# Performance work log

Hardware: AMD Instinct MI355X
Metric: run time of the kernel (lower is better)

The kernel has to match this reference:

```python
import jax, jax.numpy as jnp
import numpy as np

HIDDEN = 2048
NUM_HEADS = 16
NUM_KV_HEADS = 8
HEAD_DIM = 128
Q_SIZE = NUM_HEADS * HEAD_DIM          # 2048
KV_SIZE = NUM_KV_HEADS * HEAD_DIM      # 1024
ROPE_THETA = 1000000.0
RMS_EPS = 1e-6
SCALE = HEAD_DIM ** -0.5


def setup_inputs() -> dict:
    key = jax.random.key(0)
    k1, k2, k3 = jax.random.split(key, 3)
    T = 4096
    positions = jnp.arange(T, dtype=jnp.int64) if jax.config.jax_enable_x64 else jnp.arange(T, dtype=jnp.int32)
    hidden_states = jax.random.normal(k1, (T, HIDDEN), dtype=jnp.float32)
    qkv_w = jax.random.normal(k2, (Q_SIZE + 2 * KV_SIZE, HIDDEN), dtype=jnp.float32) * 0.02
    o_w = jax.random.normal(k3, (HIDDEN, Q_SIZE), dtype=jnp.float32) * 0.02
    q_norm_w = jnp.ones((HEAD_DIM,), dtype=jnp.float32)
    k_norm_w = jnp.ones((HEAD_DIM,), dtype=jnp.float32)
    return {
        "hidden_states": hidden_states,
        "qkv_w": qkv_w,
        "q_norm_w": q_norm_w,
        "k_norm_w": k_norm_w,
        "o_w": o_w,
        "positions": positions,
    }


def _rms_norm(x, w, eps=RMS_EPS):
    # per-head RMSNorm over last dim (head_dim)
    var = jnp.mean(jnp.square(x), axis=-1, keepdims=True)
    return x * jax.lax.rsqrt(var + eps) * w


def _rope(x, positions):
    # neox-style (rotate-half) RoPE. x: [T, H, D], positions: [T]
    D = x.shape[-1]
    inv_freq = 1.0 / (ROPE_THETA ** (jnp.arange(0, D, 2, dtype=jnp.float32) / D))  # [D/2]
    freqs = positions.astype(jnp.float32)[:, None] * inv_freq                      # [T, D/2]
    cos = jnp.cos(freqs)[:, None, :]  # [T, 1, D/2]
    sin = jnp.sin(freqs)[:, None, :]
    x1, x2 = x[..., : D // 2], x[..., D // 2 :]
    return jnp.concatenate([x1 * cos - x2 * sin, x2 * cos + x1 * sin], axis=-1)


def reference(hidden_states, qkv_w, q_norm_w, k_norm_w, o_w, positions):
    T = hidden_states.shape[0]
    qkv = hidden_states @ qkv_w.T                                   # [T, Q+2KV]
    q = qkv[:, :Q_SIZE].reshape(T, NUM_HEADS, HEAD_DIM)
    k = qkv[:, Q_SIZE : Q_SIZE + KV_SIZE].reshape(T, NUM_KV_HEADS, HEAD_DIM)
    v = qkv[:, Q_SIZE + KV_SIZE :].reshape(T, NUM_KV_HEADS, HEAD_DIM)

    # attention_bias=False path: per-head QK RMSNorm
    q = _rms_norm(q, q_norm_w)
    k = _rms_norm(k, k_norm_w)

    q = _rope(q, positions)
    k = _rope(k, positions)

    # GQA: expand KV heads to query heads
    rep = NUM_HEADS // NUM_KV_HEADS
    k = jnp.repeat(k, rep, axis=1)   # [T, H, D]
    v = jnp.repeat(v, rep, axis=1)

    scores = jnp.einsum("qhd,khd->hqk", q, k) * SCALE               # [H, T, T]
    causal = positions[:, None] >= positions[None, :]               # [T, T]
    scores = jnp.where(causal[None], scores, jnp.finfo(scores.dtype).min)
    probs = jax.nn.softmax(scores, axis=-1)
    attn = jnp.einsum("hqk,khd->qhd", probs, v)                     # [T, H, D]
    return attn.reshape(T, Q_SIZE) @ o_w.T                          # [T, HIDDEN]
```

## Files before the change

kernel.cpp:

```cpp
#include <hip/hip_runtime.h>
#include <hip/hip_bf16.h>
#include <math.h>


typedef __bf16 bf16;
typedef __bf16 bf16x4 __attribute__((ext_vector_type(4)));
typedef __bf16 bf16x8 __attribute__((ext_vector_type(8)));
typedef float  f32x4  __attribute__((ext_vector_type(4)));

__device__ __forceinline__ f32x4 mfma16(bf16x8 a, bf16x8 b, f32x4 c) {
  return __builtin_amdgcn_mfma_f32_16x16x32_bf16(a, b, c, 0, 0, 0);
}

__device__ __forceinline__ void mfma16x16_chain4(const bf16x4& a0, const bf16x4& a1,
                                                 const bf16x4& a2, const bf16x4& a3,
                                                 const bf16x4& b0, const bf16x4& b1,
                                                 const bf16x4& b2, const bf16x4& b3,
                                                 f32x4& c) {
  asm volatile(
      "s_nop 2\n\t"
      "v_mfma_f32_16x16x16_bf16 %0, %1, %5, %0\n\t"
      "v_mfma_f32_16x16x16_bf16 %0, %2, %6, %0\n\t"
      "v_mfma_f32_16x16x16_bf16 %0, %3, %7, %0\n\t"
      "v_mfma_f32_16x16x16_bf16 %0, %4, %8, %0"
      : "+v"(c)
      : "v"(a0), "v"(a1), "v"(a2), "v"(a3),
        "v"(b0), "v"(b1), "v"(b2), "v"(b3));
}

__device__ __forceinline__ void gload_lds16(const bf16* g, bf16* l) {
  __builtin_amdgcn_global_load_lds(
      (const __attribute__((address_space(1))) unsigned int*)g,
      (__attribute__((address_space(3))) unsigned int*)l, 16, 0, 0);
}

__device__ __forceinline__ void store_c(float* p, float v) { *p = v; }
__device__ __forceinline__ void store_c(bf16* p, float v) { *p = (bf16)v; }

__global__ __launch_bounds__(256) void cast_bf16(const float* __restrict__ s,
                                                 bf16* __restrict__ d) {
  int i = blockIdx.x * 256 + threadIdx.x;
  float4 a = reinterpret_cast<const float4*>(s)[i * 2];
  float4 b = reinterpret_cast<const float4*>(s)[i * 2 + 1];
  bf16x8 v = {(bf16)a.x, (bf16)a.y, (bf16)a.z, (bf16)a.w,
              (bf16)b.x, (bf16)b.y, (bf16)b.z, (bf16)b.w};
  reinterpret_cast<bf16x8*>(d)[i] = v;
}

__global__ __launch_bounds__(512, 2) void gemm8ph(const bf16* __restrict__ A,
                                                  const bf16* __restrict__ B,
                                                  bf16* __restrict__ C,
                                                  int M, int N, int K) {
  __shared__ __align__(16) bf16 As[2][256 * 64];
  __shared__ __align__(16) bf16 Bs[2][256 * 64];

  const int tid  = threadIdx.x;
  const int lane = tid & 63, wid = tid >> 6;
  const int quad = lane >> 4, l16 = lane & 15;
  const int wr = wid >> 2, wc = wid & 3;

  const int nbx = N >> 8;
  const int nwg = (M >> 8) * nbx;
  const int cpx = nwg >> 3;
  const int swz = ((int)blockIdx.x & 7) * cpx + ((int)blockIdx.x >> 3);
  const int m0 = (swz / nbx) << 8;
  const int n0 = (swz % nbx) << 8;

  const int srow = tid >> 3;
  const int scol = (((tid & 7) ^ (srow & 7)) << 3);
  const bf16* aS = &A[(size_t)(m0 + srow) * K + scol];
  const bf16* bS = &B[(size_t)(n0 + srow) * K + scol];
  const size_t rk64 = (size_t)64 * K;

  const int koff0 = ((quad)     ^ (l16 & 7)) << 3;
  const int koff1 = ((4 + quad) ^ (l16 & 7)) << 3;

  const f32x4 zero = {0.f, 0.f, 0.f, 0.f};
  f32x4 acc[8][4];
#pragma unroll
  for (int i = 0; i < 8; ++i)
#pragma unroll
    for (int j = 0; j < 4; ++j) acc[i][j] = zero;

  const int NT = K >> 6;

  {
    gload_lds16(aS,            &As[0][tid * 8]);
    gload_lds16(aS + rk64,     &As[0][4096 + tid * 8]);
    gload_lds16(aS + 2 * rk64, &As[0][8192 + tid * 8]);
    gload_lds16(aS + 3 * rk64, &As[0][12288 + tid * 8]);
    gload_lds16(bS,            &Bs[0][tid * 8]);
    gload_lds16(bS + rk64,     &Bs[0][4096 + tid * 8]);
    gload_lds16(bS + 2 * rk64, &Bs[0][8192 + tid * 8]);
    gload_lds16(bS + 3 * rk64, &Bs[0][12288 + tid * 8]);
  }
  asm volatile("s_waitcnt vmcnt(0)" ::: "memory");
  __builtin_amdgcn_s_barrier();

  for (int t = 0; t < NT; ++t) {
    const int c = t & 1;
    const bf16* AsL = As[c];
    const bf16* BsL = Bs[c];
    const bool pre = (t + 1 < NT);
    const size_t nk = (size_t)(t + 1) * 64;
    bf16* An = As[c ^ 1];
    bf16* Bn = Bs[c ^ 1];

    bf16x8 bfv[4][2];

#pragma unroll
    for (int p = 0; p < 4; ++p) {
      if (p == 0) {
#pragma unroll
        for (int fn = 0; fn < 4; ++fn) {
          const bf16* bp = &BsL[(wc * 64 + fn * 16 + l16) * 64];
          bfv[fn][0] = *reinterpret_cast<const bf16x8*>(&bp[koff0]);
          bfv[fn][1] = *reinterpret_cast<const bf16x8*>(&bp[koff1]);
        }
      }
      const bf16* ap0 = &AsL[(wr * 128 + (2 * p) * 16 + l16) * 64];
      const bf16* ap1 = ap0 + 16 * 64;
      bf16x8 a0k0 = *reinterpret_cast<const bf16x8*>(&ap0[koff0]);
      bf16x8 a0k1 = *reinterpret_cast<const bf16x8*>(&ap0[koff1]);
      bf16x8 a1k0 = *reinterpret_cast<const bf16x8*>(&ap1[koff0]);
      bf16x8 a1k1 = *reinterpret_cast<const bf16x8*>(&ap1[koff1]);

      if (p == 0 && pre) {
        gload_lds16(aS + nk,            &An[tid * 8]);
        gload_lds16(aS + rk64 + nk,     &An[4096 + tid * 8]);
        gload_lds16(aS + 2 * rk64 + nk, &An[8192 + tid * 8]);
        gload_lds16(aS + 3 * rk64 + nk, &An[12288 + tid * 8]);
      }
      if (p == 1 && pre) {
        gload_lds16(bS + nk,            &Bn[tid * 8]);
        gload_lds16(bS + rk64 + nk,     &Bn[4096 + tid * 8]);
        gload_lds16(bS + 2 * rk64 + nk, &Bn[8192 + tid * 8]);
        gload_lds16(bS + 3 * rk64 + nk, &Bn[12288 + tid * 8]);
      }

      __builtin_amdgcn_s_barrier();
      __builtin_amdgcn_sched_barrier(0);

      __builtin_amdgcn_s_setprio(1);
#pragma unroll
      for (int fn = 0; fn < 4; ++fn) {
        acc[2 * p][fn]     = mfma16(a0k1, bfv[fn][1],
                                    mfma16(a0k0, bfv[fn][0], acc[2 * p][fn]));
        acc[2 * p + 1][fn] = mfma16(a1k1, bfv[fn][1],
                                    mfma16(a1k0, bfv[fn][0], acc[2 * p + 1][fn]));
      }
      __builtin_amdgcn_s_setprio(0);

      if (p == 3 && pre) {
        asm volatile("s_waitcnt vmcnt(0)" ::: "memory");
      }
      __builtin_amdgcn_s_barrier();
    }
  }

#pragma unroll
  for (int fm = 0; fm < 8; ++fm)
#pragma unroll
    for (int fn = 0; fn < 4; ++fn)
#pragma unroll
      for (int r = 0; r < 4; ++r) {
        int row = m0 + wr * 128 + fm * 16 + quad * 4 + r;
        int col = n0 + wc * 64 + fn * 16 + l16;
        C[(size_t)row * N + col] = (bf16)acc[fm][fn][r];
      }
}

__device__ __forceinline__ void gemm_step(const bf16* AsL, const bf16* BsL,
                                          int wm, int wn, int l16, int quad,
                                          f32x4 (&acc)[4][4]) {
  bf16x8 af[4], bfr[4];
#pragma unroll
  for (int i = 0; i < 4; ++i)
    af[i] = *reinterpret_cast<const bf16x8*>(&AsL[(wm + i * 16 + l16) * 32 + quad * 8]);
#pragma unroll
  for (int j = 0; j < 4; ++j)
    bfr[j] = *reinterpret_cast<const bf16x8*>(&BsL[(wn + j * 16 + l16) * 32 + quad * 8]);
#pragma unroll
  for (int i = 0; i < 4; ++i)
#pragma unroll
    for (int j = 0; j < 4; ++j)
      acc[i][j] = mfma16(af[i], bfr[j], acc[i][j]);
}

template <typename TC>
__global__ __launch_bounds__(256, 4) void gemm_bt(const bf16* __restrict__ A,
                                                  const bf16* __restrict__ B,
                                                  TC* __restrict__ C,
                                                  int M, int N, int K) {
  __shared__ __align__(16) bf16 As[2][128 * 32];
  __shared__ __align__(16) bf16 Bs[2][128 * 32];

  const int tid  = threadIdx.x;
  const int wave = tid >> 6, lane = tid & 63;
  const int quad = lane >> 4, l16 = lane & 15;
  const int wm = (wave >> 1) * 64, wn = (wave & 1) * 64;
  const int n0 = blockIdx.x * 128, m0 = blockIdx.y * 128;

  const int r0 = tid >> 2;
  const int c0 = (tid & 3) * 8;
  const size_t aBase = (size_t)(m0 + r0) * K + c0;
  const size_t bBase = (size_t)(n0 + r0) * K + c0;
  const size_t rowK64 = (size_t)64 * K;

  const f32x4 zero = {0.f, 0.f, 0.f, 0.f};
  f32x4 acc[4][4];
#pragma unroll
  for (int i = 0; i < 4; ++i)
#pragma unroll
    for (int j = 0; j < 4; ++j) acc[i][j] = zero;

  gload_lds16(&A[aBase],          &As[0][tid * 8]);
  gload_lds16(&A[aBase + rowK64], &As[0][2048 + tid * 8]);
  gload_lds16(&B[bBase],          &Bs[0][tid * 8]);
  gload_lds16(&B[bBase + rowK64], &Bs[0][2048 + tid * 8]);
  __syncthreads();

  int cur = 0;
  for (int k0 = 32; k0 < K; k0 += 32) {
    const int nb = cur ^ 1;
    gload_lds16(&A[aBase + k0],          &As[nb][tid * 8]);
    gload_lds16(&A[aBase + rowK64 + k0], &As[nb][2048 + tid * 8]);
    gload_lds16(&B[bBase + k0],          &Bs[nb][tid * 8]);
    gload_lds16(&B[bBase + rowK64 + k0], &Bs[nb][2048 + tid * 8]);

    gemm_step(As[cur], Bs[cur], wm, wn, l16, quad, acc);

    __syncthreads();
    cur = nb;
  }
  gemm_step(As[cur], Bs[cur], wm, wn, l16, quad, acc);

#pragma unroll
  for (int i = 0; i < 4; ++i)
#pragma unroll
    for (int j = 0; j < 4; ++j)
#pragma unroll
      for (int r = 0; r < 4; ++r) {
        int row = m0 + wm + i * 16 + quad * 4 + r;
        int col = n0 + wn + j * 16 + l16;
        store_c(&C[(size_t)row * N + col], acc[i][j][r]);
      }
}

__global__ __launch_bounds__(256) void norm_rope(const bf16* __restrict__ qkv,
                                                 const float* __restrict__ qw,
                                                 const float* __restrict__ kw,
                                                 const int* __restrict__ pos,
                                                 bf16* __restrict__ qn,
                                                 bf16* __restrict__ kn) {
  const int t = blockIdx.x;
  const int wv = threadIdx.x >> 6, l = threadIdx.x & 63;

  float inv = exp2f((float)l * (-19.93156856932417f / 64.0f));
  float fr = (float)pos[t] * inv;
  float sn, cs;
  sincosf(fr, &sn, &cs);
  const float qw1 = qw[l], qw2 = qw[l + 64];
  const float kw1 = kw[l], kw2 = kw[l + 64];
  const size_t rowb = (size_t)t * 4096;

#pragma unroll
  for (int i = 0; i < 6; ++i) {
    const int h = wv * 6 + i;
    const bool isq = h < 16;
    const int col = isq ? h * 128 : 2048 + (h - 16) * 128;
    float x1 = (float)qkv[rowb + col + l];
    float x2 = (float)qkv[rowb + col + l + 64];
    float ss = x1 * x1 + x2 * x2;
#pragma unroll
    for (int o = 32; o >= 1; o >>= 1) ss += __shfl_xor(ss, o);
    float rms = rsqrtf(ss * (1.0f / 128.0f) + 1e-6f);
    float w1 = isq ? qw1 : kw1, w2 = isq ? qw2 : kw2;
    float xn1 = x1 * rms * w1, xn2 = x2 * rms * w2;
    float o1 = xn1 * cs - xn2 * sn;
    float o2 = xn2 * cs + xn1 * sn;
    if (isq) {
      qn[(size_t)t * 2048 + h * 128 + l] = (bf16)o1;
      qn[(size_t)t * 2048 + h * 128 + l + 64] = (bf16)o2;
    } else {
      kn[(size_t)t * 1024 + (h - 16) * 128 + l] = (bf16)o1;
      kn[(size_t)t * 1024 + (h - 16) * 128 + l + 64] = (bf16)o2;
    }
  }
}

__global__ __launch_bounds__(256) void transpose_v(const bf16* __restrict__ qkv,
                                                   bf16* __restrict__ vt) {
  __shared__ __align__(16) bf16 tile[128 * 72];
  const int t0 = blockIdx.x * 64, kvh = blockIdx.y;
  const int tid = threadIdx.x;
#pragma unroll
  for (int it = 0; it < 2; ++it) {
    int linear = it * 4096 + tid * 16;
    int r = linear >> 7, c = linear & 127;
    union { uint4 v; bf16 e[8]; } u0, u1;
    u0.v = *reinterpret_cast<const uint4*>(
        &qkv[(size_t)(t0 + r) * 4096 + 3072 + kvh * 128 + c]);
    u1.v = *reinterpret_cast<const uint4*>(
        &qkv[(size_t)(t0 + r) * 4096 + 3072 + kvh * 128 + c + 8]);
#pragma unroll
    for (int j = 0; j < 8; ++j) tile[(c + j) * 72 + r] = u0.e[j];
#pragma unroll
    for (int j = 0; j < 8; ++j) tile[(c + 8 + j) * 72 + r] = u1.e[j];
  }
  __syncthreads();
#pragma unroll
  for (int it = 0; it < 4; ++it) {
    int linear = it * 2048 + tid * 8;
    int d = linear >> 6, c = linear & 63;
    uint4 v = *reinterpret_cast<const uint4*>(&tile[d * 72 + c]);
    *reinterpret_cast<uint4*>(&vt[(size_t)(kvh * 128 + d) * 4096 + t0 + c]) = v;
  }
}

__global__ __launch_bounds__(256, 2) void attn(const bf16* __restrict__ q,
                                               const bf16* __restrict__ k,
                                               const bf16* __restrict__ vt,
                                               bf16* __restrict__ out) {
  __shared__ __align__(16) bf16 Ks[2][64 * 128];
  __shared__ __align__(16) bf16 Vs[2][128 * 64];

  const int head = blockIdx.y, kvh = head >> 1;
  const int bx = blockIdx.x;

  const int tid = threadIdx.x;
  const int wave = tid >> 6, lane = tid & 63;
  const int quad = lane >> 4, l16 = lane & 15;
  const float cExp = 0.08838834764831845f * 1.4426950408889634f;
  const f32x4 zero = {0.f, 0.f, 0.f, 0.f};

  int kSrc[4], vSrc[4];
#pragma unroll
  for (int it = 0; it < 4; ++it) {
    int r = (wave * 4 + it) * 4 + (lane >> 4);
    kSrc[it] = r * 1024 + kvh * 128 + (((lane & 15) ^ (r & 7)) << 3);
    int d = (wave * 4 + it) * 8 + (lane >> 3);
    vSrc[it] = (kvh * 128 + d) * 4096 + (((lane & 7) ^ (lane >> 3)) << 3);
  }

  const int kswz = (l16 & 7) << 3;
  int koff[4], voff[4];
#pragma unroll
  for (int s = 0; s < 4; ++s) {
    koff[s] = (s * 32 + quad * 8) ^ kswz;
    voff[s] = (s * 16 + quad * 4) ^ kswz;
  }

#pragma unroll
  for (int it = 0; it < 4; ++it) {
    gload_lds16(&k[kSrc[it]], &Ks[0][(wave * 4 + it) * 512]);
    gload_lds16(&vt[vSrc[it]], &Vs[0][(wave * 4 + it) * 512]);
  }
  int cur = 0;

#pragma unroll
  for (int phase = 0; phase < 2; ++phase) {
    const int qt = phase == 0 ? bx : 63 - bx;
    const int q0 = qt * 64;
    const int kend = q0 + 64;
    const int qrow = q0 + wave * 16 + l16;

    bf16x8 qf[4];
#pragma unroll
    for (int s = 0; s < 4; ++s)
      qf[s] = *reinterpret_cast<const bf16x8*>(
          &q[(size_t)qrow * 2048 + head * 128 + s * 32 + quad * 8]);

    f32x4 o_acc[8];
#pragma unroll
    for (int dt = 0; dt < 8; ++dt) o_acc[dt] = zero;
    float m_i = -3.0e38f, l_i = 0.f;

    for (int k0 = 0; k0 < kend; k0 += 64) {
      __syncthreads();

      int nk0 = -1;
      if (k0 + 64 < kend)     nk0 = k0 + 64;
      else if (phase == 0)    nk0 = 0;
      if (nk0 >= 0) {
#pragma unroll
        for (int it = 0; it < 4; ++it) {
          gload_lds16(&k[kSrc[it] + nk0 * 1024],
                      &Ks[cur ^ 1][(wave * 4 + it) * 512]);
          gload_lds16(&vt[vSrc[it] + nk0],
                      &Vs[cur ^ 1][(wave * 4 + it) * 512]);
        }
      }

      const bf16* KsL = Ks[cur];
      const bf16* VsL = Vs[cur];

      f32x4 s_acc[4];
      __builtin_amdgcn_s_setprio(1);
#pragma unroll
      for (int mt = 0; mt < 4; ++mt) {
        bf16x8 kf[4];
#pragma unroll
        for (int ks = 0; ks < 4; ++ks)
          kf[ks] = *reinterpret_cast<const bf16x8*>(
              &KsL[(mt * 16 + l16) * 128 + koff[ks]]);
        f32x4 sa = zero;
#pragma unroll
        for (int ks = 0; ks < 4; ++ks) sa = mfma16(kf[ks], qf[ks], sa);
        s_acc[mt] = sa;
      }
      __builtin_amdgcn_s_setprio(0);

      if (k0 == q0) {
        int tq = wave * 16 + l16;
#pragma unroll
        for (int mt = 0; mt < 4; ++mt)
#pragma unroll
          for (int r = 0; r < 4; ++r) {
            int tk = mt * 16 + quad * 4 + r;
            if (tk > tq) s_acc[mt][r] = -3.0e38f;
          }
      }

      {
        float mx = -3.0e38f;
#pragma unroll
        for (int mt = 0; mt < 4; ++mt)
#pragma unroll
          for (int r = 0; r < 4; ++r) mx = fmaxf(mx, s_acc[mt][r]);
        mx = fmaxf(mx, __shfl_xor(mx, 16));
        mx = fmaxf(mx, __shfl_xor(mx, 32));
        if (!__all((mx - m_i) * cExp <= 8.0f)) {
          float mn = fmaxf(m_i, mx);
          float al = exp2f((m_i - mn) * cExp);
          m_i = mn;
          l_i *= al;
#pragma unroll
          for (int dt = 0; dt < 8; ++dt)
#pragma unroll
            for (int r = 0; r < 4; ++r) o_acc[dt][r] *= al;
        }
        float nmc = -m_i * cExp;
        float rs = 0.f;
#pragma unroll
        for (int mt = 0; mt < 4; ++mt)
#pragma unroll
          for (int r = 0; r < 4; ++r) {
            float pe = exp2f(fmaf(s_acc[mt][r], cExp, nmc));
            s_acc[mt][r] = pe;
            rs += pe;
          }
        rs += __shfl_xor(rs, 16);
        rs += __shfl_xor(rs, 32);
        l_i += rs;
      }

      bf16x4 pb[4];
#pragma unroll
      for (int mt = 0; mt < 4; ++mt) {
        bf16x4 t;
#pragma unroll
        for (int r = 0; r < 4; ++r) t[r] = (bf16)s_acc[mt][r];
        pb[mt] = t;
      }

      __builtin_amdgcn_s_setprio(1);
#pragma unroll
      for (int dt = 0; dt < 8; ++dt) {
        const bf16* vrow = &VsL[(dt * 16 + l16) * 64];
        bf16x4 va0 = *reinterpret_cast<const bf16x4*>(&vrow[voff[0]]);
        bf16x4 va1 = *reinterpret_cast<const bf16x4*>(&vrow[voff[1]]);
        bf16x4 va2 = *reinterpret_cast<const bf16x4*>(&vrow[voff[2]]);
        bf16x4 va3 = *reinterpret_cast<const bf16x4*>(&vrow[voff[3]]);
        mfma16x16_chain4(va0, va1, va2, va3, pb[0], pb[1], pb[2], pb[3],
                         o_acc[dt]);
      }
      __builtin_amdgcn_s_setprio(0);
      cur ^= 1;
    }

    float rl = __builtin_amdgcn_rcpf(l_i);
#pragma unroll
    for (int dt = 0; dt < 8; ++dt) {
      bf16x4 ov;
#pragma unroll
      for (int r = 0; r < 4; ++r) ov[r] = (bf16)(o_acc[dt][r] * rl);
      *reinterpret_cast<bf16x4*>(
          &out[(size_t)qrow * 2048 + head * 128 + dt * 16 + quad * 4]) = ov;
    }
  }
}

extern "C" void kernel_launch(void* const* d_in, const int* in_sizes, int n_in,
                              void* d_out, int out_size, void* d_ws, size_t ws_size,
                              hipStream_t stream) {
  const float* hidden = (const float*)d_in[0];
  const float* qkv_w  = (const float*)d_in[1];
  const float* qnw    = (const float*)d_in[2];
  const float* knw    = (const float*)d_in[3];
  const float* o_w    = (const float*)d_in[4];
  const int*   pos    = (const int*)d_in[5];

  bf16* qkv = (bf16*)d_ws;
  bf16* qn  = qkv + (size_t)4096 * 4096;
  bf16* kn  = qn  + (size_t)4096 * 2048;
  bf16* vt  = kn  + (size_t)4096 * 1024;
  bf16* ao  = vt  + (size_t)1024 * 4096;
  bf16* hb  = ao;
  bf16* wq  = kn;
  bf16* wo  = qn;
  float* out = (float*)d_out;

  cast_bf16<<<4096, 256, 0, stream>>>(hidden, hb);
  cast_bf16<<<4096, 256, 0, stream>>>(qkv_w, wq);
  gemm8ph<<<256, 512, 0, stream>>>(hb, wq, qkv, 4096, 4096, 2048);
  norm_rope<<<4096, 256, 0, stream>>>(qkv, qnw, knw, pos, qn, kn);
  transpose_v<<<dim3(64, 8), 256, 0, stream>>>(qkv, vt);
  attn<<<dim3(32, 16), 256, 0, stream>>>(qn, kn, vt, ao);
  cast_bf16<<<2048, 256, 0, stream>>>(o_w, wo);
  gemm_bt<<<dim3(16, 32), 256, 0, stream>>>(ao, wo, out, 4096, 2048, 2048);
}
```

Baseline: 399.1 us.

## Restructure attention to 128-row query tiles with 8 waves sharing K/V loads

Changes the attention kernel from 256-thread blocks that each process two paired 64-row query tiles to 512-thread blocks that each process one 128-row query tile, with 8 waves sharing every K/V tile staged in shared memory. This halves the K/V global-to-LDS traffic per query row. Blocks are ordered longest-first (heavy tiles scheduled first) in a flat 1D grid, with the head as the fast index. The per-wave causal mask now applies on the diagonal tiles. The trade-off is causal imbalance within a block: waves with earlier rows compute fully masked tiles. Load balance now relies on scheduling order instead of pairing tiles.

```diff
diff --git a/kernel.cpp b/kernel.cpp
--- a/kernel.cpp
+++ b/kernel.cpp
@@ -318,15 +318,20 @@
   }
 }
 
-__global__ __launch_bounds__(256, 2) void attn(const bf16* __restrict__ q,
+__global__ __launch_bounds__(512, 4) void attn(const bf16* __restrict__ q,
                                                const bf16* __restrict__ k,
                                                const bf16* __restrict__ vt,
                                                bf16* __restrict__ out) {
   __shared__ __align__(16) bf16 Ks[2][64 * 128];
   __shared__ __align__(16) bf16 Vs[2][128 * 64];
 
-  const int head = blockIdx.y, kvh = head >> 1;
-  const int bx = blockIdx.x;
+  const int bx   = blockIdx.x;
+  const int slot = bx >> 4;
+  const int head = bx & 15;
+  const int kvh  = head >> 1;
+  const int qt   = slot < 16 ? 31 - slot : slot - 16;
+  const int q0   = qt * 128;
+  const int kend = q0 + 128;
 
   const int tid = threadIdx.x;
   const int wave = tid >> 6, lane = tid & 63;
@@ -334,13 +339,13 @@
   const float cExp = 0.08838834764831845f * 1.4426950408889634f;
   const f32x4 zero = {0.f, 0.f, 0.f, 0.f};
 
-  int kSrc[4], vSrc[4];
-#pragma unroll
-  for (int it = 0; it < 4; ++it) {
-    int r = (wave * 4 + it) * 4 + (lane >> 4);
+  int kSrc[2], vSrc[2];
+#pragma unroll
+  for (int it = 0; it < 2; ++it) {
+    int r = it * 32 + wave * 4 + (lane >> 4);
     kSrc[it] = r * 1024 + kvh * 128 + (((lane & 15) ^ (r & 7)) << 3);
-    int d = (wave * 4 + it) * 8 + (lane >> 3);
-    vSrc[it] = (kvh * 128 + d) * 4096 + (((lane & 7) ^ (lane >> 3)) << 3);
+    int d = it * 64 + wave * 8 + (lane >> 3);
+    vSrc[it] = (kvh * 128 + d) * 4096 + (((lane & 7) ^ ((lane >> 3) & 7)) << 3);
   }
 
   const int kswz = (l16 & 7) << 3;
@@ -352,142 +357,133 @@
   }
 
 #pragma unroll
-  for (int it = 0; it < 4; ++it) {
-    gload_lds16(&k[kSrc[it]], &Ks[0][(wave * 4 + it) * 512]);
-    gload_lds16(&vt[vSrc[it]], &Vs[0][(wave * 4 + it) * 512]);
+  for (int it = 0; it < 2; ++it) {
+    gload_lds16(&k[kSrc[it]], &Ks[0][it * 4096 + wave * 512]);
+    gload_lds16(&vt[vSrc[it]], &Vs[0][it * 4096 + wave * 512]);
   }
   int cur = 0;
 
-#pragma unroll
-  for (int phase = 0; phase < 2; ++phase) {
-    const int qt = phase == 0 ? bx : 63 - bx;
-    const int q0 = qt * 64;
-    const int kend = q0 + 64;
-    const int qrow = q0 + wave * 16 + l16;
-
-    bf16x8 qf[4];
-#pragma unroll
-    for (int s = 0; s < 4; ++s)
-      qf[s] = *reinterpret_cast<const bf16x8*>(
-          &q[(size_t)qrow * 2048 + head * 128 + s * 32 + quad * 8]);
-
-    f32x4 o_acc[8];
-#pragma unroll
-    for (int dt = 0; dt < 8; ++dt) o_acc[dt] = zero;
-    float m_i = -3.0e38f, l_i = 0.f;
-
-    for (int k0 = 0; k0 < kend; k0 += 64) {
-      __syncthreads();
-
-      int nk0 = -1;
-      if (k0 + 64 < kend)     nk0 = k0 + 64;
-      else if (phase == 0)    nk0 = 0;
-      if (nk0 >= 0) {
-#pragma unroll
-        for (int it = 0; it < 4; ++it) {
-          gload_lds16(&k[kSrc[it] + nk0 * 1024],
-                      &Ks[cur ^ 1][(wave * 4 + it) * 512]);
-          gload_lds16(&vt[vSrc[it] + nk0],
-                      &Vs[cur ^ 1][(wave * 4 + it) * 512]);
+  const int qrow = q0 + wave * 16 + l16;
+
+  bf16x8 qf[4];
+#pragma unroll
+  for (int s = 0; s < 4; ++s)
+    qf[s] = *reinterpret_cast<const bf16x8*>(
+        &q[(size_t)qrow * 2048 + head * 128 + s * 32 + quad * 8]);
+
+  f32x4 o_acc[8];
+#pragma unroll
+  for (int dt = 0; dt < 8; ++dt) o_acc[dt] = zero;
+  float m_i = -3.0e38f, l_i = 0.f;
+
+  for (int k0 = 0; k0 < kend; k0 += 64) {
+    __syncthreads();
+
+    if (k0 + 64 < kend) {
+#pragma unroll
+      for (int it = 0; it < 2; ++it) {
+        gload_lds16(&k[kSrc[it] + (k0 + 64) * 1024],
+                    &Ks[cur ^ 1][it * 4096 + wave * 512]);
+        gload_lds16(&vt[vSrc[it] + (k0 + 64)],
+                    &Vs[cur ^ 1][it * 4096 + wave * 512]);
+      }
+    }
+
+    const bf16* KsL = Ks[cur];
+    const bf16* VsL = Vs[cur];
+
+    f32x4 s_acc[4];
+    __builtin_amdgcn_s_setprio(1);
+#pragma unroll
+    for (int mt = 0; mt < 4; ++mt) {
+      bf16x8 kf[4];
+#pragma unroll
+      for (int ks = 0; ks < 4; ++ks)
+        kf[ks] = *reinterpret_cast<const bf16x8*>(
+            &KsL[(mt * 16 + l16) * 128 + koff[ks]]);
+      f32x4 sa = zero;
+#pragma unroll
+      for (int ks = 0; ks < 4; ++ks) sa = mfma16(kf[ks], qf[ks], sa);
+      s_acc[mt] = sa;
+    }
+    __builtin_amdgcn_s_setprio(0);
+
+    if (k0 + 64 > q0 + wave * 16) {
+      const int tq = qrow;
+#pragma unroll
+      for (int mt = 0; mt < 4; ++mt)
+#pragma unroll
+        for (int r = 0; r < 4; ++r) {
+          int tk = k0 + mt * 16 + quad * 4 + r;
+          if (tk > tq) s_acc[mt][r] = -3.0e38f;
         }
-      }
-
-      const bf16* KsL = Ks[cur];
-      const bf16* VsL = Vs[cur];
-
-      f32x4 s_acc[4];
-      __builtin_amdgcn_s_setprio(1);
-#pragma unroll
-      for (int mt = 0; mt < 4; ++mt) {
-        bf16x8 kf[4];
-#pragma unroll
-        for (int ks = 0; ks < 4; ++ks)
-          kf[ks] = *reinterpret_cast<const bf16x8*>(
-              &KsL[(mt * 16 + l16) * 128 + koff[ks]]);
-        f32x4 sa = zero;
-#pragma unroll
-        for (int ks = 0; ks < 4; ++ks) sa = mfma16(kf[ks], qf[ks], sa);
-        s_acc[mt] = sa;
-      }
-      __builtin_amdgcn_s_setprio(0);
-
-      if (k0 == q0) {
-        int tq = wave * 16 + l16;
-#pragma unroll
-        for (int mt = 0; mt < 4; ++mt)
-#pragma unroll
-          for (int r = 0; r < 4; ++r) {
-            int tk = mt * 16 + quad * 4 + r;
-            if (tk > tq) s_acc[mt][r] = -3.0e38f;
-          }
-      }
-
-      {
-        float mx = -3.0e38f;
-#pragma unroll
-        for (int mt = 0; mt < 4; ++mt)
-#pragma unroll
-          for (int r = 0; r < 4; ++r) mx = fmaxf(mx, s_acc[mt][r]);
-        mx = fmaxf(mx, __shfl_xor(mx, 16));
-        mx = fmaxf(mx, __shfl_xor(mx, 32));
-        if (!__all((mx - m_i) * cExp <= 8.0f)) {
-          float mn = fmaxf(m_i, mx);
-          float al = exp2f((m_i - mn) * cExp);
-          m_i = mn;
-          l_i *= al;
-#pragma unroll
-          for (int dt = 0; dt < 8; ++dt)
-#pragma unroll
-            for (int r = 0; r < 4; ++r) o_acc[dt][r] *= al;
+    }
+
+    {
+      float mx = -3.0e38f;
+#pragma unroll
+      for (int mt = 0; mt < 4; ++mt)
+#pragma unroll
+        for (int r = 0; r < 4; ++r) mx = fmaxf(mx, s_acc[mt][r]);
+      mx = fmaxf(mx, __shfl_xor(mx, 16));
+      mx = fmaxf(mx, __shfl_xor(mx, 32));
+      if (!__all((mx - m_i) * cExp <= 8.0f)) {
+        float mn = fmaxf(m_i, mx);
+        float al = exp2f((m_i - mn) * cExp);
+        m_i = mn;
+        l_i *= al;
+#pragma unroll
+        for (int dt = 0; dt < 8; ++dt)
+#pragma unroll
+          for (int r = 0; r < 4; ++r) o_acc[dt][r] *= al;
+      }
+      float nmc = -m_i * cExp;
+      float rs = 0.f;
+#pragma unroll
+      for (int mt = 0; mt < 4; ++mt)
+#pragma unroll
+        for (int r = 0; r < 4; ++r) {
+          float pe = exp2f(fmaf(s_acc[mt][r], cExp, nmc));
+          s_acc[mt][r] = pe;
+          rs += pe;
         }
-        float nmc = -m_i * cExp;
-        float rs = 0.f;
-#pragma unroll
-        for (int mt = 0; mt < 4; ++mt)
-#pragma unroll
-          for (int r = 0; r < 4; ++r) {
-            float pe = exp2f(fmaf(s_acc[mt][r], cExp, nmc));
-            s_acc[mt][r] = pe;
-            rs += pe;
-          }
-        rs += __shfl_xor(rs, 16);
-        rs += __shfl_xor(rs, 32);
-        l_i += rs;
-      }
-
-      bf16x4 pb[4];
-#pragma unroll
-      for (int mt = 0; mt < 4; ++mt) {
-        bf16x4 t;
-#pragma unroll
-        for (int r = 0; r < 4; ++r) t[r] = (bf16)s_acc[mt][r];
-        pb[mt] = t;
-      }
-
-      __builtin_amdgcn_s_setprio(1);
-#pragma unroll
-      for (int dt = 0; dt < 8; ++dt) {
-        const bf16* vrow = &VsL[(dt * 16 + l16) * 64];
-        bf16x4 va0 = *reinterpret_cast<const bf16x4*>(&vrow[voff[0]]);
-        bf16x4 va1 = *reinterpret_cast<const bf16x4*>(&vrow[voff[1]]);
-        bf16x4 va2 = *reinterpret_cast<const bf16x4*>(&vrow[voff[2]]);
-        bf16x4 va3 = *reinterpret_cast<const bf16x4*>(&vrow[voff[3]]);
-        mfma16x16_chain4(va0, va1, va2, va3, pb[0], pb[1], pb[2], pb[3],
-                         o_acc[dt]);
-      }
-      __builtin_amdgcn_s_setprio(0);
-      cur ^= 1;
-    }
-
-    float rl = __builtin_amdgcn_rcpf(l_i);
+      rs += __shfl_xor(rs, 16);
+      rs += __shfl_xor(rs, 32);
+      l_i += rs;
+    }
+
+    bf16x4 pb[4];
+#pragma unroll
+    for (int mt = 0; mt < 4; ++mt) {
+      bf16x4 t;
+#pragma unroll
+      for (int r = 0; r < 4; ++r) t[r] = (bf16)s_acc[mt][r];
+      pb[mt] = t;
+    }
+
+    __builtin_amdgcn_s_setprio(1);
 #pragma unroll
     for (int dt = 0; dt < 8; ++dt) {
-      bf16x4 ov;
-#pragma unroll
-      for (int r = 0; r < 4; ++r) ov[r] = (bf16)(o_acc[dt][r] * rl);
-      *reinterpret_cast<bf16x4*>(
-          &out[(size_t)qrow * 2048 + head * 128 + dt * 16 + quad * 4]) = ov;
-    }
+      const bf16* vrow = &VsL[(dt * 16 + l16) * 64];
+      bf16x4 va0 = *reinterpret_cast<const bf16x4*>(&vrow[voff[0]]);
+      bf16x4 va1 = *reinterpret_cast<const bf16x4*>(&vrow[voff[1]]);
+      bf16x4 va2 = *reinterpret_cast<const bf16x4*>(&vrow[voff[2]]);
+      bf16x4 va3 = *reinterpret_cast<const bf16x4*>(&vrow[voff[3]]);
+      mfma16x16_chain4(va0, va1, va2, va3, pb[0], pb[1], pb[2], pb[3],
+                       o_acc[dt]);
+    }
+    __builtin_amdgcn_s_setprio(0);
+    cur ^= 1;
+  }
+
+  float rl = __builtin_amdgcn_rcpf(l_i);
+#pragma unroll
+  for (int dt = 0; dt < 8; ++dt) {
+    bf16x4 ov;
+#pragma unroll
+    for (int r = 0; r < 4; ++r) ov[r] = (bf16)(o_acc[dt][r] * rl);
+    *reinterpret_cast<bf16x4*>(
+        &out[(size_t)qrow * 2048 + head * 128 + dt * 16 + quad * 4]) = ov;
   }
 }
 
@@ -516,7 +512,7 @@
   gemm8ph<<<256, 512, 0, stream>>>(hb, wq, qkv, 4096, 4096, 2048);
   norm_rope<<<4096, 256, 0, stream>>>(qkv, qnw, knw, pos, qn, kn);
   transpose_v<<<dim3(64, 8), 256, 0, stream>>>(qkv, vt);
-  attn<<<dim3(32, 16), 256, 0, stream>>>(qn, kn, vt, ao);
+  attn<<<512, 512, 0, stream>>>(qn, kn, vt, ao);
   cast_bf16<<<2048, 256, 0, stream>>>(o_w, wo);
   gemm_bt<<<dim3(16, 32), 256, 0, stream>>>(ao, wo, out, 4096, 2048, 2048);
 }
```

New measurement: 407.0 us. Within noise of the previous version (+2.0%).
